# Kernel tuning notes

Measured on AMD Instinct MI355X. Metric: run time of the kernel, lower is better.

The kernel has to match this reference:

```python
import jax, jax.numpy as jnp
import numpy as np

B = 4        # samples
GP = 6       # graphs per sample (K*2)
N = 1024     # nodes per graph
DIN = 128    # input feature dim
D = 128      # out_channels
E = 16384    # edges per graph


def setup_inputs() -> dict:
    k = jax.random.split(jax.random.key(0), 10)
    G = B * GP
    s = 0.05
    return {
        "x": jax.random.normal(k[0], (G, N, DIN), jnp.float32),
        "edge_attr": jax.random.uniform(k[1], (G, E, 6), jnp.float32),
        "gcn_W": jax.random.normal(k[2], (4, DIN, D), jnp.float32) * s,
        "gcn_b": jnp.zeros((4, D), jnp.float32),
        "Ws": jax.random.normal(k[3], (4, D, D), jnp.float32) * s,
        "lin1_W": jax.random.normal(k[4], (GP * D, 20), jnp.float32) * s,
        "lin1_b": jnp.zeros((20,), jnp.float32),
        "codefc_W": jax.random.normal(k[5], (20, 2), jnp.float32) * s,
        "codefc_b": jnp.zeros((2,), jnp.float32),
        "lin2_W": jax.random.normal(k[6], (GP * D, GP), jnp.float32) * s,
        "lin2_b": jnp.zeros((GP,), jnp.float32),
        "simfc_W": jax.random.normal(k[7], (GP, 2), jnp.float32) * s,
        "simfc_b": jnp.zeros((2,), jnp.float32),
        "edge_index": jax.random.randint(k[8], (G, 2, E), 0, N, jnp.int64),
    }


def _gcn(x, src, dst, ew, W, b):
    # PyG GCNConv with normalize=True, add_self_loops=True (self-loop weight 1)
    n = x.shape[0]
    deg = jax.ops.segment_sum(ew, dst, num_segments=n) + 1.0
    dinv = jax.lax.rsqrt(deg)
    xw = x @ W
    norm = dinv[src] * ew * dinv[dst]               # [E]
    agg = jax.ops.segment_sum(norm[:, None] * xw[src], dst, num_segments=n)
    return agg + (dinv * dinv)[:, None] * xw + b    # self-loop term + bias


def _gnnlayer(x, ei, ea, gcn_W, gcn_b, Ws):
    # x_tmp = sum_i relu(GCN_i(x, ew=edge_attr[:, i+2])) @ Ws[i]
    src, dst = ei[0], ei[1]
    def chan(W, b, Wmix, ew):
        return jnp.maximum(_gcn(x, src, dst, ew, W, b), 0.0) @ Wmix
    return jax.vmap(chan)(gcn_W, gcn_b, Ws, ea[:, 2:6].T).sum(0)  # [N, D]


def _forward(x, edge_attr, gcn_W, gcn_b, Ws, lin1_W, lin1_b, codefc_W,
             codefc_b, lin2_W, lin2_b, simfc_W, simfc_b, edge_index):
    # per-graph GNN layer over all G = B*GP graphs
    x_tmp = jax.vmap(lambda xg, eig, eag: _gnnlayer(xg, eig, eag, gcn_W, gcn_b, Ws))(
        x, edge_index, edge_attr)                    # [G, N, D]
    g = x_tmp.mean(axis=1).reshape(B, GP * D)        # g_matrix [B, 768]
    # L2-normalize rows (F.normalize eps=1e-12)
    xn = x_tmp / jnp.clip(jnp.linalg.norm(x_tmp, axis=-1, keepdims=True), 1e-12)
    xn = xn.reshape(B, GP, N, D)
    # all-pairs cosine sim -> tanh -> 21-bin histogram on [-1, 1] -> weighted sum
    S = jnp.tanh(jnp.einsum('bind,bjmd->bijnm', xn, xn))   # [B,GP,GP,N,N]
    idx = jnp.clip(jnp.floor((S + 1.0) * (21.0 / 2.0)).astype(jnp.int32), 0, 20)
    centers = jnp.linspace(-1.0, 1.0, 21, dtype=jnp.float32)
    # hist/(N*N) dot centers == mean of per-element bin centers
    sim = centers[idx].mean(axis=(3, 4))             # [B, GP, GP]
    # backnet
    feat = jnp.maximum(g @ lin1_W + lin1_b, 0.0)     # feature_of_G [B, 20]
    code = jax.nn.log_softmax(feat @ codefc_W + codefc_b, axis=1)
    strength = g @ lin2_W + lin2_b                   # [B, GP]
    sim_res = jax.nn.log_softmax((sim.mean(axis=2) * strength) @ simfc_W + simfc_b, axis=1)
    r = 0.4 * code + 0.6 * sim_res
    return r, feat


def reference(x, edge_attr, gcn_W, gcn_b, Ws, lin1_W, lin1_b, codefc_W,
              codefc_b, lin2_W, lin2_b, simfc_W, simfc_b, edge_index):
    return _forward(x, edge_attr, gcn_W, gcn_b, Ws, lin1_W, lin1_b, codefc_W,
                    codefc_b, lin2_W, lin2_b, simfc_W, simfc_b, edge_index)
```

## Files before the change

### kernel.cpp

```cpp
#include <hip/hip_runtime.h>

#define NG 24
#define NB 4
#define GPg 6
#define NN 1024
#define DD 128
#define EE 16384

typedef __bf16 bf16;
typedef __bf16 bf16x8 __attribute__((ext_vector_type(8)));
typedef float f32x4 __attribute__((ext_vector_type(4)));

#define GLOBAL_AS __attribute__((address_space(1)))
#define LDS_AS __attribute__((address_space(3)))

__global__ void k_wconv(const float* __restrict__ gW, const float* __restrict__ Ws,
                        bf16* __restrict__ gwt, bf16* __restrict__ wst) {
  int i = blockIdx.x * 256 + threadIdx.x;
  int c = i >> 14, k = (i >> 7) & 127, j = i & 127;
  gwt[(c << 14) | (j << 7) | k] = (bf16)gW[i];
  wst[(j << 9) | (c << 7) | k] = (bf16)Ws[i];
}

__global__ void k_hist(const int* __restrict__ ei, int* __restrict__ counts) {
  int t = blockIdx.x * 256 + threadIdx.x;
  if (t >= NG * EE) return;
  int g = t >> 14, e = t & (EE - 1);
  int dst = ei[g * 2 * EE + EE + e];
  atomicAdd(&counts[g * NN + dst], 1);
}

__global__ void k_scan(const int* __restrict__ counts, int* __restrict__ offs,
                       int* __restrict__ cursor) {
  __shared__ int sh[NN];
  int g = blockIdx.x, t = threadIdx.x;
  int myc = counts[g * NN + t];
  sh[t] = myc;
  __syncthreads();
  for (int d2 = 1; d2 < NN; d2 <<= 1) {
    int v = (t >= d2) ? sh[t - d2] : 0;
    __syncthreads();
    sh[t] += v;
    __syncthreads();
  }
  int incl = sh[t];
  int excl = incl - myc;
  offs[g * 1025 + t] = excl;
  cursor[g * NN + t] = excl;
  if (t == NN - 1) offs[g * 1025 + NN] = incl;
}

__global__ void k_scatter(const int* __restrict__ ei, const float* __restrict__ ea,
                          int* __restrict__ cursor, int* __restrict__ csrs,
                          float* __restrict__ csre) {
  int t = blockIdx.x * 256 + threadIdx.x;
  if (t >= NG * EE) return;
  int g = t >> 14, e = t & (EE - 1);
  int src = ei[g * 2 * EE + e], dst = ei[g * 2 * EE + EE + e];
  int pos = atomicAdd(&cursor[g * NN + dst], 1);
  size_t idx = (size_t)g * EE + pos;
  csrs[idx] = src;
  const float* p = ea + ((size_t)g * EE + e) * 6;
#pragma unroll
  for (int c = 0; c < 4; c++) csre[idx * 4 + c] = p[2 + c];
}

__global__ void k_deg(const int* __restrict__ offs, const float* __restrict__ csre,
                      float* __restrict__ dinv4) {
  int t = blockIdx.x * 256 + threadIdx.x;
  int c = t & 3, n = (t >> 2) & (NN - 1), g = t >> 12;
  int beg = offs[g * 1025 + n], end = offs[g * 1025 + n + 1];
  const float* ep = csre + (size_t)g * EE * 4 + c;
  float s = 1.0f;
  for (int p = beg; p < end; ++p) s += ep[(size_t)p * 4];
  dinv4[t] = rsqrtf(s);
}

__global__ __launch_bounds__(256) void k_xw(const float* __restrict__ x,
                                            const bf16* __restrict__ gwt,
                                            const float* __restrict__ dinv4,
                                            bf16* __restrict__ xw) {
  int bid = blockIdx.x;
  int gc = bid >> 3, mb = bid & 7;
  int g = gc >> 2, c = gc & 3;
  int lane = threadIdx.x & 63, wid = threadIdx.x >> 6;
  int wm = wid >> 1, wn = wid & 1;
  int row0 = mb * 128 + wm * 64, col0 = wn * 64;
  const float* A = x + (size_t)g * NN * DD;
  const bf16* Bt = gwt + (size_t)c * DD * DD;
  int lr = lane & 15, lk = (lane >> 4) * 8;
  f32x4 acc[4][4] = {};
  for (int kc = 0; kc < 128; kc += 32) {
    bf16x8 a[4], b[4];
#pragma unroll
    for (int i2 = 0; i2 < 4; i2++) {
      const f32x4* pa = (const f32x4*)(A + (size_t)(row0 + i2 * 16 + lr) * DD + kc + lk);
      f32x4 f0 = pa[0], f1 = pa[1];
#pragma unroll
      for (int q = 0; q < 4; q++) { a[i2][q] = (bf16)f0[q]; a[i2][4 + q] = (bf16)f1[q]; }
    }
#pragma unroll
    for (int j2 = 0; j2 < 4; j2++)
      b[j2] = *(const bf16x8*)(Bt + (size_t)(col0 + j2 * 16 + lr) * DD + kc + lk);
#pragma unroll
    for (int i2 = 0; i2 < 4; i2++)
#pragma unroll
      for (int j2 = 0; j2 < 4; j2++)
        acc[i2][j2] = __builtin_amdgcn_mfma_f32_16x16x32_bf16(a[i2], b[j2], acc[i2][j2], 0, 0, 0);
  }
  bf16* out = xw + (size_t)g * NN * 512 + c * 128;
  const float* dv = dinv4 + ((size_t)g * NN) * 4 + c;
  int cr = (lane >> 4) * 4, cc = lane & 15;
#pragma unroll
  for (int i2 = 0; i2 < 4; i2++)
#pragma unroll
    for (int r2 = 0; r2 < 4; r2++) {
      int row = row0 + i2 * 16 + cr + r2;
      float dvv = dv[row * 4];
#pragma unroll
      for (int j2 = 0; j2 < 4; j2++)
        out[(size_t)row * 512 + col0 + j2 * 16 + cc] = (bf16)(acc[i2][j2][r2] * dvv);
    }
}

__global__ __launch_bounds__(256) void k_agg(const int* __restrict__ offs, const int* __restrict__ csrs,
                                             const float* __restrict__ csre, const float* __restrict__ dinv4,
                                             const float* __restrict__ gb, const bf16* __restrict__ xw,
                                             bf16* __restrict__ hb) {
  int bid = blockIdx.x;
  int lb = (bid & 7) * (NG * 256 / 8) + (bid >> 3);
  int g = lb >> 8, n4 = lb & 255;
  int wid = threadIdx.x >> 6, lane = threadIdx.x & 63;
  int n = n4 * 4 + wid;
  int c = lane >> 4, d0 = (lane & 15) * 8;
  const bf16* xwg = xw + (size_t)g * NN * 512;
  int beg = offs[g * 1025 + n], end = offs[g * 1025 + n + 1];
  const int* sp = csrs + (size_t)g * EE;
  const float* ep = csre + (size_t)g * EE * 4;
  float dvn = dinv4[((size_t)g * NN + n) * 4 + c];
  float acc[8] = {};
  int p = beg;
  for (; p + 1 < end; p += 2) {
    int s0 = sp[p], s1 = sp[p + 1];
    float w0 = ep[(size_t)p * 4 + c];
    float w1 = ep[(size_t)(p + 1) * 4 + c];
    bf16x8 v0 = *(const bf16x8*)(xwg + (size_t)s0 * 512 + lane * 8);
    bf16x8 v1 = *(const bf16x8*)(xwg + (size_t)s1 * 512 + lane * 8);
#pragma unroll
    for (int q = 0; q < 8; q++) acc[q] += w0 * (float)v0[q];
#pragma unroll
    for (int q = 0; q < 8; q++) acc[q] += w1 * (float)v1[q];
  }
  if (p < end) {
    int s0 = sp[p];
    float w0 = ep[(size_t)p * 4 + c];
    bf16x8 v0 = *(const bf16x8*)(xwg + (size_t)s0 * 512 + lane * 8);
#pragma unroll
    for (int q = 0; q < 8; q++) acc[q] += w0 * (float)v0[q];
  }
  bf16x8 vs = *(const bf16x8*)(xwg + (size_t)n * 512 + lane * 8);
  bf16x8 o;
#pragma unroll
  for (int q = 0; q < 8; q++) {
    float r2 = dvn * (acc[q] + (float)vs[q]) + gb[c * 128 + d0 + q];
    o[q] = (bf16)fmaxf(r2, 0.f);
  }
  *(bf16x8*)(hb + ((size_t)g * NN + n) * 512 + lane * 8) = o;
}

__global__ __launch_bounds__(256) void k_mixn(const bf16* __restrict__ hb,
                                              const bf16* __restrict__ wst,
                                              float* __restrict__ gmat,
                                              bf16* __restrict__ xn) {
  __shared__ float rowssq[128];
  int bid = blockIdx.x;
  int g = bid >> 3, mb = bid & 7;
  int lane = threadIdx.x & 63, wid = threadIdx.x >> 6;
  int wm = wid >> 1, wn = wid & 1;
  int row0 = mb * 128 + wm * 64, col0 = wn * 64;
  const bf16* H = hb + (size_t)g * NN * 512;
  int lr = lane & 15, lk = (lane >> 4) * 8;
  if (threadIdx.x < 128) rowssq[threadIdx.x] = 0.f;
  f32x4 acc[4][4] = {};
  for (int kc = 0; kc < 512; kc += 32) {
    bf16x8 a[4], b[4];
#pragma unroll
    for (int i2 = 0; i2 < 4; i2++)
      a[i2] = *(const bf16x8*)(H + (size_t)(row0 + i2 * 16 + lr) * 512 + kc + lk);
#pragma unroll
    for (int j2 = 0; j2 < 4; j2++)
      b[j2] = *(const bf16x8*)(wst + (size_t)(col0 + j2 * 16 + lr) * 512 + kc + lk);
#pragma unroll
    for (int i2 = 0; i2 < 4; i2++)
#pragma unroll
      for (int j2 = 0; j2 < 4; j2++)
        acc[i2][j2] = __builtin_amdgcn_mfma_f32_16x16x32_bf16(a[i2], b[j2], acc[i2][j2], 0, 0, 0);
  }
  __syncthreads();
  int cr = (lane >> 4) * 4, cc = lane & 15;
#pragma unroll
  for (int i2 = 0; i2 < 4; i2++)
#pragma unroll
    for (int r2 = 0; r2 < 4; r2++) {
      float s = 0.f;
#pragma unroll
      for (int j2 = 0; j2 < 4; j2++) { float v = acc[i2][j2][r2]; s += v * v; }
#pragma unroll
      for (int d2 = 1; d2 < 16; d2 <<= 1) s += __shfl_xor(s, d2);
      if (cc == 0) atomicAdd(&rowssq[wm * 64 + i2 * 16 + cr + r2], s);
    }
#pragma unroll
  for (int j2 = 0; j2 < 4; j2++) {
    float s = 0.f;
#pragma unroll
    for (int i2 = 0; i2 < 4; i2++)
#pragma unroll
      for (int r2 = 0; r2 < 4; r2++) s += acc[i2][j2][r2];
    s += __shfl_xor(s, 16);
    s += __shfl_xor(s, 32);
    if ((lane >> 4) == 0)
      atomicAdd(&gmat[(g / GPg) * 768 + (g % GPg) * 128 + col0 + j2 * 16 + cc], s * (1.0f / NN));
  }
  __syncthreads();
  bf16* xp = xn + (size_t)g * NN * DD;
#pragma unroll
  for (int i2 = 0; i2 < 4; i2++)
#pragma unroll
    for (int r2 = 0; r2 < 4; r2++) {
      int rowl = wm * 64 + i2 * 16 + cr + r2;
      float inv = 1.0f / fmaxf(sqrtf(rowssq[rowl]), 1e-12f);
#pragma unroll
      for (int j2 = 0; j2 < 4; j2++)
        xp[(size_t)(mb * 128 + rowl) * DD + col0 + j2 * 16 + cc] = (bf16)(acc[i2][j2][r2] * inv);
    }
}

__global__ __launch_bounds__(256, 4) void k_pair(const bf16* __restrict__ xn,
                                                 unsigned* __restrict__ simsum) {
  __shared__ char lds[32768];
  int bid = blockIdx.x;
  int lb = (bid & 7) * 168 + (bid >> 3);
  int b = lb / 336, rem = lb % 336;
  int pj = rem >> 4, rem2 = rem & 15;
  int s128 = rem2 >> 1, half = rem2 & 1;
  int r = pj, i = 0;
  while (r >= 6 - i) { r -= 6 - i; ++i; }
  int j = i + r;
  bool isdiag = (i == j);
  int tb = half * 8, te = tb + 8;
  if (isdiag && 2 * s128 > tb) tb = 2 * s128;
  if (tb >= te) return;
  int lane = threadIdx.x & 63, wid = threadIdx.x >> 6;
  int lr = lane & 15, hi16 = (lane >> 4) * 16;
  const char* Ag = (const char*)(xn + ((size_t)(b * GPg + i) * NN + s128 * 128 + wid * 32) * DD);
  const char* Bg0 = (const char*)(xn + (size_t)(b * GPg + j) * NN * DD);

  bf16x8 a[2][4];
#pragma unroll
  for (int g2 = 0; g2 < 2; g2++)
#pragma unroll
    for (int kc = 0; kc < 4; kc++) {
      a[g2][kc] = *(const bf16x8*)(Ag + (g2 * 16 + lr) * 256 + kc * 64 + hi16);
      asm volatile("" :: "v"(a[g2][kc]));
    }

  int gofs = (wid * 16 + lr) * 256 + hi16;
  auto stage = [&](int buf, int tn) {
    const char* src = Bg0 + tn * 16384 + gofs;
#pragma unroll
    for (int u = 0; u < 4; ++u)
      __builtin_amdgcn_global_load_lds((const GLOBAL_AS void*)(src + u * 64),
                                       (LDS_AS void*)(lds + buf * 16384 + u * 4096 + wid * 1024),
                                       16, 0, 0);
  };
  stage(0, tb);
  if (tb + 1 < te) stage(1, tb + 1);

  int cnt = 0;
  int cc = lane & 15, cr = (lane >> 4) * 4;
  for (int t = tb; t < te; ++t) {
    int cur = (t - tb) & 1;
    if (t < te - 1) asm volatile("s_waitcnt vmcnt(4)" ::: "memory");
    else            asm volatile("s_waitcnt vmcnt(0)" ::: "memory");
    __builtin_amdgcn_s_barrier();
    const char* Bl = lds + cur * 16384;
    f32x4 acc[2][4] = {};
#pragma unroll
    for (int kc = 0; kc < 4; kc++) {
      bf16x8 bb[4];
#pragma unroll
      for (int j2 = 0; j2 < 4; j2++)
        bb[j2] = *(const bf16x8*)(Bl + kc * 4096 + j2 * 1024 + lane * 16);
#pragma unroll
      for (int g2 = 0; g2 < 2; g2++)
#pragma unroll
        for (int j2 = 0; j2 < 4; j2++)
          acc[g2][j2] = __builtin_amdgcn_mfma_f32_16x16x32_bf16(a[g2][kc], bb[j2], acc[g2][j2], 0, 0, 0);
    }
    asm volatile("s_waitcnt lgkmcnt(0)" ::: "memory");
    __builtin_amdgcn_sched_barrier(0);
    __builtin_amdgcn_s_barrier();
    if (t + 2 < te) stage(cur, t + 2);
    if (isdiag && t < 2 * s128 + 2) {
      int tc = 0;
#pragma unroll
      for (int g2 = 0; g2 < 2; g2++)
#pragma unroll
        for (int j2 = 0; j2 < 4; j2++)
#pragma unroll
          for (int r2 = 0; r2 < 4; r2++) {
            float v = acc[g2][j2][r2];
            float e = __builtin_amdgcn_exp2f(v * 2.8853900817779268f);
            int idx = (int)(21.f - 21.f * __builtin_amdgcn_rcpf(e + 1.f));
            int lm = t * 64 + j2 * 16 + cc;
            int ln = s128 * 128 + wid * 32 + g2 * 16 + cr + r2;
            tc += (lm > ln) ? 2 * idx : (lm == ln ? idx : 0);
          }
      cnt += tc;
    } else {
      int tc = 0;
#pragma unroll
      for (int g2 = 0; g2 < 2; g2++)
#pragma unroll
        for (int j2 = 0; j2 < 4; j2++)
#pragma unroll
          for (int r2 = 0; r2 < 4; r2++) {
            float v = acc[g2][j2][r2];
            float e = __builtin_amdgcn_exp2f(v * 2.8853900817779268f);
            tc += (int)(21.f - 21.f * __builtin_amdgcn_rcpf(e + 1.f));
          }
      cnt += isdiag ? 2 * tc : tc;
    }
  }
#pragma unroll
  for (int d2 = 32; d2; d2 >>= 1) cnt += __shfl_xor(cnt, d2);
  if (lane == 0) atomicAdd(&simsum[((size_t)b * GPg + i) * GPg + j], (unsigned)cnt);
}

__global__ void k_back(const float* __restrict__ gmat, const unsigned* __restrict__ simsum,
                       const float* __restrict__ l1W, const float* __restrict__ l1b,
                       const float* __restrict__ cfW, const float* __restrict__ cfb,
                       const float* __restrict__ l2W, const float* __restrict__ l2b,
                       const float* __restrict__ sfW, const float* __restrict__ sfb,
                       float* __restrict__ out) {
  __shared__ float feat[NB][20];
  __shared__ float strength[NB][GPg];
  __shared__ float simmean[NB][GPg];
  int t = threadIdx.x, g = t >> 3, l = t & 7;
  if (g < 80) {
    int b = g / 20, jj = g % 20;
    float s = 0.f;
#pragma unroll 8
    for (int k = l; k < 768; k += 8) s += gmat[b * 768 + k] * l1W[k * 20 + jj];
    s += __shfl_xor(s, 1); s += __shfl_xor(s, 2); s += __shfl_xor(s, 4);
    if (l == 0) {
      float f = fmaxf(s + l1b[jj], 0.f);
      feat[b][jj] = f;
      out[8 + b * 20 + jj] = f;
    }
  } else if (g < 104) {
    int q = g - 80, b = q / GPg, pp = q % GPg;
    float s = 0.f;
#pragma unroll 8
    for (int k = l; k < 768; k += 8) s += gmat[b * 768 + k] * l2W[k * GPg + pp];
    s += __shfl_xor(s, 1); s += __shfl_xor(s, 2); s += __shfl_xor(s, 4);
    if (l == 0) strength[b][pp] = s + l2b[pp];
  } else if (t >= 832 && t < 856) {
    int q = t - 832; int b = q / GPg, ii = q % GPg;
    float s = 0.f;
    for (int jj = 0; jj < GPg; jj++) {
      int lo = ii < jj ? ii : jj, hi = ii < jj ? jj : ii;
      s += -1.0f + 0.1f * (float)simsum[(b * GPg + lo) * GPg + hi] * (1.0f / (1024.f * 1024.f));
    }
    simmean[b][ii] = s * (1.0f / GPg);
  }
  __syncthreads();
  if (t < NB) {
    int b = t;
    float l1v[2], l2v[2];
#pragma unroll
    for (int u = 0; u < 2; u++) {
      float s = cfb[u];
      for (int jj = 0; jj < 20; jj++) s += feat[b][jj] * cfW[jj * 2 + u];
      l1v[u] = s;
      float s2 = sfb[u];
      for (int pp = 0; pp < GPg; pp++) s2 += simmean[b][pp] * strength[b][pp] * sfW[pp * 2 + u];
      l2v[u] = s2;
    }
    float m1 = fmaxf(l1v[0], l1v[1]);
    float lse1 = m1 + logf(expf(l1v[0] - m1) + expf(l1v[1] - m1));
    float m2 = fmaxf(l2v[0], l2v[1]);
    float lse2 = m2 + logf(expf(l2v[0] - m2) + expf(l2v[1] - m2));
    out[b * 2 + 0] = 0.4f * (l1v[0] - lse1) + 0.6f * (l2v[0] - lse2);
    out[b * 2 + 1] = 0.4f * (l1v[1] - lse1) + 0.6f * (l2v[1] - lse2);
  }
}

extern "C" void kernel_launch(void* const* d_in, const int* in_sizes, int n_in,
                              void* d_out, int out_size, void* d_ws, size_t ws_size,
                              hipStream_t stream) {
  const float* x   = (const float*)d_in[0];
  const float* ea  = (const float*)d_in[1];
  const float* gW  = (const float*)d_in[2];
  const float* gb  = (const float*)d_in[3];
  const float* Ws  = (const float*)d_in[4];
  const float* l1W = (const float*)d_in[5];
  const float* l1b = (const float*)d_in[6];
  const float* cfW = (const float*)d_in[7];
  const float* cfb = (const float*)d_in[8];
  const float* l2W = (const float*)d_in[9];
  const float* l2b = (const float*)d_in[10];
  const float* sfW = (const float*)d_in[11];
  const float* sfb = (const float*)d_in[12];
  const int* eidx  = (const int*)d_in[13];
  float* out = (float*)d_out;

  char* w = (char*)d_ws;
  auto alloc = [&](size_t bytes) { char* p = w; w += (bytes + 255) & ~(size_t)255; return (void*)p; };
  bf16* gwt     = (bf16*)alloc(4 * DD * DD * 2);
  bf16* wst     = (bf16*)alloc(4 * DD * DD * 2);
  int* counts   = (int*)alloc((size_t)NG * NN * 4);
  float* dinv4  = (float*)alloc((size_t)NG * NN * 4 * 4);
  int* offs     = (int*)alloc((size_t)NG * 1025 * 4);
  int* cursor   = (int*)alloc((size_t)NG * NN * 4);
  int* csrs     = (int*)alloc((size_t)NG * EE * 4);
  float* csre   = (float*)alloc((size_t)NG * EE * 4 * 4);
  bf16* xw      = (bf16*)alloc((size_t)NG * NN * 512 * 2);
  bf16* hb      = (bf16*)alloc((size_t)NG * NN * 512 * 2);
  float* gmat   = (float*)alloc((size_t)NB * 768 * 4);
  unsigned* simsum = (unsigned*)alloc((size_t)NB * 36 * 4);
  bf16* xn      = (bf16*)alloc((size_t)NG * NN * DD * 2 + 16384);

  hipMemsetAsync(counts, 0, (size_t)NG * NN * 4, stream);
  hipMemsetAsync(gmat, 0, 12288 + 576, stream);

  k_wconv<<<256, 256, 0, stream>>>(gW, Ws, gwt, wst);
  k_hist<<<(NG * EE) / 256, 256, 0, stream>>>(eidx, counts);
  k_scan<<<NG, 1024, 0, stream>>>(counts, offs, cursor);
  k_scatter<<<(NG * EE) / 256, 256, 0, stream>>>(eidx, ea, cursor, csrs, csre);
  k_deg<<<(NG * NN * 4) / 256, 256, 0, stream>>>(offs, csre, dinv4);
  k_xw<<<NG * 4 * 8, 256, 0, stream>>>(x, gwt, dinv4, xw);
  k_agg<<<NG * 256, 256, 0, stream>>>(offs, csrs, csre, dinv4, gb, xw, hb);
  k_mixn<<<NG * 8, 256, 0, stream>>>(hb, wst, gmat, xn);
  k_pair<<<1344, 256, 0, stream>>>(xn, simsum);
  k_back<<<1, 1024, 0, stream>>>(gmat, simsum, l1W, l1b, cfW, cfb, l2W, l2b, sfW, sfb, out);
}
```

Measured before the change: 186.5 us.

## Drop LDS staging in pair kernel; each wave streams B tiles directly from global

The all-pairs similarity kernel no longer stages B tiles through LDS with global_load_lds double buffering and barriers. Each wave now owns a 32-row A strip and loads 32-column B tiles straight from global/L2 into registers. Diagonal work is skipped per wave starting at its own tile, and the grid is halved. This removes barrier and LDS traffic but gives up B reuse across the four waves, so global/L2 load traffic rises and latency hiding now relies on unroll and occupancy. Load balance across waves on diagonal blocks also becomes uneven.

```diff
diff --git a/kernel.cpp b/kernel.cpp
--- a/kernel.cpp
+++ b/kernel.cpp
@@ -237,83 +237,62 @@
 
 __global__ __launch_bounds__(256, 4) void k_pair(const bf16* __restrict__ xn,
                                                  unsigned* __restrict__ simsum) {
-  __shared__ char lds[32768];
   int bid = blockIdx.x;
-  int lb = (bid & 7) * 168 + (bid >> 3);
-  int b = lb / 336, rem = lb % 336;
-  int pj = rem >> 4, rem2 = rem & 15;
-  int s128 = rem2 >> 1, half = rem2 & 1;
+  int lb = (bid & 7) * 84 + (bid >> 3);
+  int b = lb / 168, rem = lb % 168;
+  int pj = rem >> 3, rsg = rem & 7;
+  int lane = threadIdx.x & 63, wid = threadIdx.x >> 6;
+  int rs = rsg * 4 + wid;
   int r = pj, i = 0;
   while (r >= 6 - i) { r -= 6 - i; ++i; }
   int j = i + r;
   bool isdiag = (i == j);
-  int tb = half * 8, te = tb + 8;
-  if (isdiag && 2 * s128 > tb) tb = 2 * s128;
-  if (tb >= te) return;
-  int lane = threadIdx.x & 63, wid = threadIdx.x >> 6;
+  int tb = isdiag ? rs : 0;
   int lr = lane & 15, hi16 = (lane >> 4) * 16;
-  const char* Ag = (const char*)(xn + ((size_t)(b * GPg + i) * NN + s128 * 128 + wid * 32) * DD);
-  const char* Bg0 = (const char*)(xn + (size_t)(b * GPg + j) * NN * DD);
+  const char* Ag = (const char*)(xn + (size_t)(b * GPg + i) * NN * DD)
+                   + (rs * 32 + lr) * 256 + hi16;
+  const char* Bg = (const char*)(xn + (size_t)(b * GPg + j) * NN * DD)
+                   + lr * 256 + hi16;
 
   bf16x8 a[2][4];
 #pragma unroll
   for (int g2 = 0; g2 < 2; g2++)
 #pragma unroll
-    for (int kc = 0; kc < 4; kc++) {
-      a[g2][kc] = *(const bf16x8*)(Ag + (g2 * 16 + lr) * 256 + kc * 64 + hi16);
-      asm volatile("" :: "v"(a[g2][kc]));
-    }
-
-  int gofs = (wid * 16 + lr) * 256 + hi16;
-  auto stage = [&](int buf, int tn) {
-    const char* src = Bg0 + tn * 16384 + gofs;
-#pragma unroll
-    for (int u = 0; u < 4; ++u)
-      __builtin_amdgcn_global_load_lds((const GLOBAL_AS void*)(src + u * 64),
-                                       (LDS_AS void*)(lds + buf * 16384 + u * 4096 + wid * 1024),
-                                       16, 0, 0);
-  };
-  stage(0, tb);
-  if (tb + 1 < te) stage(1, tb + 1);
+    for (int kc = 0; kc < 4; kc++)
+      a[g2][kc] = *(const bf16x8*)(Ag + g2 * 4096 + kc * 64);
 
   int cnt = 0;
-  int cc = lane & 15, cr = (lane >> 4) * 4;
-  for (int t = tb; t < te; ++t) {
-    int cur = (t - tb) & 1;
-    if (t < te - 1) asm volatile("s_waitcnt vmcnt(4)" ::: "memory");
-    else            asm volatile("s_waitcnt vmcnt(0)" ::: "memory");
-    __builtin_amdgcn_s_barrier();
-    const char* Bl = lds + cur * 16384;
-    f32x4 acc[2][4] = {};
-#pragma unroll
-    for (int kc = 0; kc < 4; kc++) {
-      bf16x8 bb[4];
-#pragma unroll
-      for (int j2 = 0; j2 < 4; j2++)
-        bb[j2] = *(const bf16x8*)(Bl + kc * 4096 + j2 * 1024 + lane * 16);
+  int cc = lr, cr = (lane >> 4) * 4;
+#pragma unroll 2
+  for (int t = tb; t < 32; ++t) {
+    const char* Bt = Bg + t * 8192;
+    bf16x8 bb[2][4];
+#pragma unroll
+    for (int j2 = 0; j2 < 2; j2++)
+#pragma unroll
+      for (int kc = 0; kc < 4; kc++)
+        bb[j2][kc] = *(const bf16x8*)(Bt + j2 * 4096 + kc * 64);
+    f32x4 acc[2][2] = {};
+#pragma unroll
+    for (int kc = 0; kc < 4; kc++)
 #pragma unroll
       for (int g2 = 0; g2 < 2; g2++)
 #pragma unroll
-        for (int j2 = 0; j2 < 4; j2++)
-          acc[g2][j2] = __builtin_amdgcn_mfma_f32_16x16x32_bf16(a[g2][kc], bb[j2], acc[g2][j2], 0, 0, 0);
-    }
-    asm volatile("s_waitcnt lgkmcnt(0)" ::: "memory");
-    __builtin_amdgcn_sched_barrier(0);
-    __builtin_amdgcn_s_barrier();
-    if (t + 2 < te) stage(cur, t + 2);
-    if (isdiag && t < 2 * s128 + 2) {
+        for (int j2 = 0; j2 < 2; j2++)
+          acc[g2][j2] = __builtin_amdgcn_mfma_f32_16x16x32_bf16(a[g2][kc], bb[j2][kc], acc[g2][j2], 0, 0, 0);
+    if (isdiag && t == rs) {
       int tc = 0;
 #pragma unroll
       for (int g2 = 0; g2 < 2; g2++)
 #pragma unroll
-        for (int j2 = 0; j2 < 4; j2++)
+        for (int j2 = 0; j2 < 2; j2++)
 #pragma unroll
           for (int r2 = 0; r2 < 4; r2++) {
             float v = acc[g2][j2][r2];
             float e = __builtin_amdgcn_exp2f(v * 2.8853900817779268f);
             int idx = (int)(21.f - 21.f * __builtin_amdgcn_rcpf(e + 1.f));
-            int lm = t * 64 + j2 * 16 + cc;
-            int ln = s128 * 128 + wid * 32 + g2 * 16 + cr + r2;
+            int lm = j2 * 16 + cc;
+            int ln = g2 * 16 + cr + r2;
             tc += (lm > ln) ? 2 * idx : (lm == ln ? idx : 0);
           }
       cnt += tc;
@@ -322,7 +301,7 @@
 #pragma unroll
       for (int g2 = 0; g2 < 2; g2++)
 #pragma unroll
-        for (int j2 = 0; j2 < 4; j2++)
+        for (int j2 = 0; j2 < 2; j2++)
 #pragma unroll
           for (int r2 = 0; r2 < 4; r2++) {
             float v = acc[g2][j2][r2];
@@ -429,7 +408,7 @@
   bf16* hb      = (bf16*)alloc((size_t)NG * NN * 512 * 2);
   float* gmat   = (float*)alloc((size_t)NB * 768 * 4);
   unsigned* simsum = (unsigned*)alloc((size_t)NB * 36 * 4);
-  bf16* xn      = (bf16*)alloc((size_t)NG * NN * DD * 2 + 16384);
+  bf16* xn      = (bf16*)alloc((size_t)NG * NN * DD * 2);
 
   hipMemsetAsync(counts, 0, (size_t)NG * NN * 4, stream);
   hipMemsetAsync(gmat, 0, 12288 + 576, stream);
@@ -442,6 +421,6 @@
   k_xw<<<NG * 4 * 8, 256, 0, stream>>>(x, gwt, dinv4, xw);
   k_agg<<<NG * 256, 256, 0, stream>>>(offs, csrs, csre, dinv4, gb, xw, hb);
   k_mixn<<<NG * 8, 256, 0, stream>>>(hb, wst, gmat, xn);
-  k_pair<<<1344, 256, 0, stream>>>(xn, simsum);
+  k_pair<<<672, 256, 0, stream>>>(xn, simsum);
   k_back<<<1, 1024, 0, stream>>>(gmat, simsum, l1W, l1b, cfW, cfb, l2W, l2b, sfW, sfb, out);
 }
```

Result: slower. 235.1 us (+26.1%).

## Fuse degree sums into histogram pass, merge weight convert, shrink pair tile

Applied to the files above, without the earlier changes.

Merges the weight-conversion kernel into the edge-histogram kernel and accumulates per-node edge-weight degree sums there with float atomics. The rsqrt degree normalisation moves into the scan kernel, so the separate k_deg pass is removed. k_pair now stages 32-column B tiles instead of 64, halving LDS use and the accumulator count per iteration while doubling the iteration count. This cuts launches and a CSR re-read, at the cost of many float atomics and nondeterministic summation order in the degree sums.

```diff
diff --git a/kernel.cpp b/kernel.cpp
--- a/kernel.cpp
+++ b/kernel.cpp
@@ -14,28 +14,40 @@
 #define GLOBAL_AS __attribute__((address_space(1)))
 #define LDS_AS __attribute__((address_space(3)))
 
-__global__ void k_wconv(const float* __restrict__ gW, const float* __restrict__ Ws,
+__global__ void k_histw(const int* __restrict__ ei, const float* __restrict__ ea,
+                        int* __restrict__ counts, float* __restrict__ degsum,
+                        const float* __restrict__ gW, const float* __restrict__ Ws,
                         bf16* __restrict__ gwt, bf16* __restrict__ wst) {
-  int i = blockIdx.x * 256 + threadIdx.x;
-  int c = i >> 14, k = (i >> 7) & 127, j = i & 127;
-  gwt[(c << 14) | (j << 7) | k] = (bf16)gW[i];
-  wst[(j << 9) | (c << 7) | k] = (bf16)Ws[i];
-}
-
-__global__ void k_hist(const int* __restrict__ ei, int* __restrict__ counts) {
-  int t = blockIdx.x * 256 + threadIdx.x;
-  if (t >= NG * EE) return;
+  int bid = blockIdx.x;
+  if (bid >= 1536) {
+    int i = (bid - 1536) * 256 + threadIdx.x;
+    int c = i >> 14, k = (i >> 7) & 127, j = i & 127;
+    gwt[(c << 14) | (j << 7) | k] = (bf16)gW[i];
+    wst[(j << 9) | (c << 7) | k] = (bf16)Ws[i];
+    return;
+  }
+  int t = bid * 256 + threadIdx.x;
   int g = t >> 14, e = t & (EE - 1);
   int dst = ei[g * 2 * EE + EE + e];
   atomicAdd(&counts[g * NN + dst], 1);
+  const float* p = ea + ((size_t)g * EE + e) * 6;
+  float* ds = degsum + (((size_t)g << 10) + dst) * 4;
+#pragma unroll
+  for (int c = 0; c < 4; c++) atomicAdd(&ds[c], p[2 + c]);
 }
 
 __global__ void k_scan(const int* __restrict__ counts, int* __restrict__ offs,
-                       int* __restrict__ cursor) {
+                       int* __restrict__ cursor, const float* __restrict__ degsum,
+                       float* __restrict__ dinv4) {
   __shared__ int sh[NN];
   int g = blockIdx.x, t = threadIdx.x;
   int myc = counts[g * NN + t];
   sh[t] = myc;
+  f32x4 ds = *(const f32x4*)(degsum + ((size_t)g * NN + t) * 4);
+  f32x4 dv;
+#pragma unroll
+  for (int c = 0; c < 4; c++) dv[c] = rsqrtf(ds[c] + 1.0f);
+  *(f32x4*)(dinv4 + ((size_t)g * NN + t) * 4) = dv;
   __syncthreads();
   for (int d2 = 1; d2 < NN; d2 <<= 1) {
     int v = (t >= d2) ? sh[t - d2] : 0;
@@ -63,17 +75,6 @@
   const float* p = ea + ((size_t)g * EE + e) * 6;
 #pragma unroll
   for (int c = 0; c < 4; c++) csre[idx * 4 + c] = p[2 + c];
-}
-
-__global__ void k_deg(const int* __restrict__ offs, const float* __restrict__ csre,
-                      float* __restrict__ dinv4) {
-  int t = blockIdx.x * 256 + threadIdx.x;
-  int c = t & 3, n = (t >> 2) & (NN - 1), g = t >> 12;
-  int beg = offs[g * 1025 + n], end = offs[g * 1025 + n + 1];
-  const float* ep = csre + (size_t)g * EE * 4 + c;
-  float s = 1.0f;
-  for (int p = beg; p < end; ++p) s += ep[(size_t)p * 4];
-  dinv4[t] = rsqrtf(s);
 }
 
 __global__ __launch_bounds__(256) void k_xw(const float* __restrict__ x,
@@ -237,7 +238,7 @@
 
 __global__ __launch_bounds__(256, 4) void k_pair(const bf16* __restrict__ xn,
                                                  unsigned* __restrict__ simsum) {
-  __shared__ char lds[32768];
+  __shared__ char lds[16384];
   int bid = blockIdx.x;
   int lb = (bid & 7) * 168 + (bid >> 3);
   int b = lb / 336, rem = lb % 336;
@@ -247,8 +248,8 @@
   while (r >= 6 - i) { r -= 6 - i; ++i; }
   int j = i + r;
   bool isdiag = (i == j);
-  int tb = half * 8, te = tb + 8;
-  if (isdiag && 2 * s128 > tb) tb = 2 * s128;
+  int tb = half * 16, te = tb + 16;
+  if (isdiag && 4 * s128 > tb) tb = 4 * s128;
   if (tb >= te) return;
   int lane = threadIdx.x & 63, wid = threadIdx.x >> 6;
   int lr = lane & 15, hi16 = (lane >> 4) * 16;
@@ -264,14 +265,13 @@
       asm volatile("" :: "v"(a[g2][kc]));
     }
 
-  int gofs = (wid * 16 + lr) * 256 + hi16;
   auto stage = [&](int buf, int tn) {
-    const char* src = Bg0 + tn * 16384 + gofs;
-#pragma unroll
-    for (int u = 0; u < 4; ++u)
-      __builtin_amdgcn_global_load_lds((const GLOBAL_AS void*)(src + u * 64),
-                                       (LDS_AS void*)(lds + buf * 16384 + u * 4096 + wid * 1024),
-                                       16, 0, 0);
+    const char* src = Bg0 + tn * 8192;
+#pragma unroll
+    for (int j2 = 0; j2 < 2; ++j2)
+      __builtin_amdgcn_global_load_lds(
+          (const GLOBAL_AS void*)(src + (j2 * 16 + lr) * 256 + wid * 64 + hi16),
+          (LDS_AS void*)(lds + buf * 8192 + wid * 2048 + j2 * 1024), 16, 0, 0);
   };
   stage(0, tb);
   if (tb + 1 < te) stage(1, tb + 1);
@@ -280,39 +280,39 @@
   int cc = lane & 15, cr = (lane >> 4) * 4;
   for (int t = tb; t < te; ++t) {
     int cur = (t - tb) & 1;
-    if (t < te - 1) asm volatile("s_waitcnt vmcnt(4)" ::: "memory");
+    if (t < te - 1) asm volatile("s_waitcnt vmcnt(2)" ::: "memory");
     else            asm volatile("s_waitcnt vmcnt(0)" ::: "memory");
     __builtin_amdgcn_s_barrier();
-    const char* Bl = lds + cur * 16384;
-    f32x4 acc[2][4] = {};
+    const char* Bl = lds + cur * 8192;
+    f32x4 acc[2][2] = {};
 #pragma unroll
     for (int kc = 0; kc < 4; kc++) {
-      bf16x8 bb[4];
-#pragma unroll
-      for (int j2 = 0; j2 < 4; j2++)
-        bb[j2] = *(const bf16x8*)(Bl + kc * 4096 + j2 * 1024 + lane * 16);
+      bf16x8 bb[2];
+#pragma unroll
+      for (int j2 = 0; j2 < 2; j2++)
+        bb[j2] = *(const bf16x8*)(Bl + kc * 2048 + j2 * 1024 + lane * 16);
 #pragma unroll
       for (int g2 = 0; g2 < 2; g2++)
 #pragma unroll
-        for (int j2 = 0; j2 < 4; j2++)
+        for (int j2 = 0; j2 < 2; j2++)
           acc[g2][j2] = __builtin_amdgcn_mfma_f32_16x16x32_bf16(a[g2][kc], bb[j2], acc[g2][j2], 0, 0, 0);
     }
     asm volatile("s_waitcnt lgkmcnt(0)" ::: "memory");
     __builtin_amdgcn_sched_barrier(0);
     __builtin_amdgcn_s_barrier();
     if (t + 2 < te) stage(cur, t + 2);
-    if (isdiag && t < 2 * s128 + 2) {
+    if (isdiag && t < 4 * s128 + 4) {
       int tc = 0;
 #pragma unroll
       for (int g2 = 0; g2 < 2; g2++)
 #pragma unroll
-        for (int j2 = 0; j2 < 4; j2++)
+        for (int j2 = 0; j2 < 2; j2++)
 #pragma unroll
           for (int r2 = 0; r2 < 4; r2++) {
             float v = acc[g2][j2][r2];
             float e = __builtin_amdgcn_exp2f(v * 2.8853900817779268f);
             int idx = (int)(21.f - 21.f * __builtin_amdgcn_rcpf(e + 1.f));
-            int lm = t * 64 + j2 * 16 + cc;
+            int lm = t * 32 + j2 * 16 + cc;
             int ln = s128 * 128 + wid * 32 + g2 * 16 + cr + r2;
             tc += (lm > ln) ? 2 * idx : (lm == ln ? idx : 0);
           }
@@ -322,7 +322,7 @@
 #pragma unroll
       for (int g2 = 0; g2 < 2; g2++)
 #pragma unroll
-        for (int j2 = 0; j2 < 4; j2++)
+        for (int j2 = 0; j2 < 2; j2++)
 #pragma unroll
           for (int r2 = 0; r2 < 4; r2++) {
             float v = acc[g2][j2][r2];
@@ -419,6 +419,7 @@
   auto alloc = [&](size_t bytes) { char* p = w; w += (bytes + 255) & ~(size_t)255; return (void*)p; };
   bf16* gwt     = (bf16*)alloc(4 * DD * DD * 2);
   bf16* wst     = (bf16*)alloc(4 * DD * DD * 2);
+  float* degsum = (float*)alloc((size_t)NG * NN * 4 * 4);
   int* counts   = (int*)alloc((size_t)NG * NN * 4);
   float* dinv4  = (float*)alloc((size_t)NG * NN * 4 * 4);
   int* offs     = (int*)alloc((size_t)NG * 1025 * 4);
@@ -429,16 +430,14 @@
   bf16* hb      = (bf16*)alloc((size_t)NG * NN * 512 * 2);
   float* gmat   = (float*)alloc((size_t)NB * 768 * 4);
   unsigned* simsum = (unsigned*)alloc((size_t)NB * 36 * 4);
-  bf16* xn      = (bf16*)alloc((size_t)NG * NN * DD * 2 + 16384);
-
-  hipMemsetAsync(counts, 0, (size_t)NG * NN * 4, stream);
+  bf16* xn      = (bf16*)alloc((size_t)NG * NN * DD * 2);
+
+  hipMemsetAsync(degsum, 0, (size_t)NG * NN * 16 + (size_t)NG * NN * 4, stream);
   hipMemsetAsync(gmat, 0, 12288 + 576, stream);
 
-  k_wconv<<<256, 256, 0, stream>>>(gW, Ws, gwt, wst);
-  k_hist<<<(NG * EE) / 256, 256, 0, stream>>>(eidx, counts);
-  k_scan<<<NG, 1024, 0, stream>>>(counts, offs, cursor);
+  k_histw<<<1792, 256, 0, stream>>>(eidx, ea, counts, degsum, gW, Ws, gwt, wst);
+  k_scan<<<NG, 1024, 0, stream>>>(counts, offs, cursor, degsum, dinv4);
   k_scatter<<<(NG * EE) / 256, 256, 0, stream>>>(eidx, ea, cursor, csrs, csre);
-  k_deg<<<(NG * NN * 4) / 256, 256, 0, stream>>>(offs, csre, dinv4);
   k_xw<<<NG * 4 * 8, 256, 0, stream>>>(x, gwt, dinv4, xw);
   k_agg<<<NG * 256, 256, 0, stream>>>(offs, csrs, csre, dinv4, gb, xw, hb);
   k_mixn<<<NG * 8, 256, 0, stream>>>(hb, wst, gmat, xn);
```

Measured after the change: 249.0 us. +33.5%, slower.
